# Kernel tuning notes

Hardware: AMD Instinct MI355X
Metric: run time of the kernel (lower is better)

The kernel has to match this reference:

```python
import jax, jax.numpy as jnp
import numpy as np

B, T, F, H = 64, 2048, 128, 32  # batch, seq_len, input_features, lstm hidden


def setup_inputs() -> dict:
    key = jax.random.key(0)
    ks = jax.random.split(key, 4)
    X = jax.random.normal(ks[0], (B, T, F), dtype=jnp.float32)
    # combined gate weights, order (i, f, g, o) as in flax.linen.LSTMCell
    Wx = jax.random.normal(ks[1], (F, 4 * H), dtype=jnp.float32) / np.float32(np.sqrt(F))
    Wh = jax.random.normal(ks[2], (H, 4 * H), dtype=jnp.float32) / np.float32(np.sqrt(H))
    b = jnp.zeros((4 * H,), dtype=jnp.float32)
    Wd = jax.random.normal(ks[3], (H, 1), dtype=jnp.float32) / np.float32(np.sqrt(H))
    bd = jnp.zeros((1,), dtype=jnp.float32)
    return {"X": X, "Wx": Wx, "Wh": Wh, "b": b, "Wd": Wd, "bd": bd}


def reference(X, Wx, Wh, b, Wd, bd):
    # Precompute input->gate projections for all timesteps in one GEMM.
    xg = jnp.einsum('btf,fg->btg', X, Wx) + b  # [B, T, 4H]

    def step(carry, xg_t):
        c, h = carry
        g = xg_t + h @ Wh  # [B, 4H]
        i, f, gc, o = jnp.split(g, 4, axis=-1)
        c = jax.nn.sigmoid(f) * c + jax.nn.sigmoid(i) * jnp.tanh(gc)
        h = jax.nn.sigmoid(o) * jnp.tanh(c)
        return (c, h), None

    zeros = jnp.zeros((X.shape[0], H), X.dtype)
    (c_T, h_T), _ = jax.lax.scan(step, (zeros, zeros), jnp.swapaxes(xg, 0, 1))
    # Dense(1) applied to outputs, then last timestep selected == Dense on h_T
    return h_T @ Wd + bd  # [B, 1]
```

## Files before the change

### kernel.cpp

```cpp
#include <hip/hip_runtime.h>
#include <math.h>

#define BB 64
#define TT 2048
#define FF 128
#define HH 32
#define GG 128

#define S1f (-1.4426950408889634f)
#define S2f (-2.8853900817779268f)

typedef _Float16 half2_t __attribute__((ext_vector_type(2)));

__device__ __forceinline__ unsigned h2u(half2_t v) {
    unsigned u; __builtin_memcpy(&u, &v, 4); return u;
}
__device__ __forceinline__ half2_t u2h(unsigned u) {
    half2_t v; __builtin_memcpy(&v, &u, 4); return v;
}
__device__ __forceinline__ half2_t pkrtz(float a, float b) {
    auto r = __builtin_amdgcn_cvt_pkrtz(a, b);
    half2_t v; __builtin_memcpy(&v, &r, 4); return v;
}
__device__ __forceinline__ float rcp_(float x) { return __builtin_amdgcn_rcpf(x); }
__device__ __forceinline__ float exp2_(float x) { return __builtin_amdgcn_exp2f(x); }

#define DPP_(x, ctrl) \
    ((unsigned)__builtin_amdgcn_mov_dpp((int)(x), (ctrl), 0xF, 0xF, true))
#define CTRL_XOR1 0xB1
#define CTRL_XOR2 0x4E
#define CTRL_ROR4 0x124
#define CTRL_ROR8 0x128
#define SWZ16_(x) ((unsigned)__builtin_amdgcn_ds_swizzle((int)(x), 0x401F))

#if __has_builtin(__builtin_amdgcn_permlane16_swap)
#define HAVE_PL16 1
#else
#define HAVE_PL16 0
#endif

__device__ __forceinline__ void gather_tree(unsigned v0, unsigned g[16]) {
    unsigned v1 = DPP_(v0, CTRL_XOR2);
#if HAVE_PL16
    auto sw = __builtin_amdgcn_permlane16_swap(v0, v1, false, false);
    unsigned s0 = (unsigned)sw[0], s1 = (unsigned)sw[1];
    g[0] = s0;
    g[1] = s1;
    g[2] = DPP_(s0, CTRL_XOR2);
    g[3] = DPP_(s1, CTRL_XOR2);
#else
    g[0] = v0;
    g[1] = v1;
    g[2] = SWZ16_(v0);
    g[3] = SWZ16_(v1);
#endif
#pragma unroll
    for (int r = 0; r < 4; ++r) g[4 + r] = DPP_(g[r], CTRL_ROR4);
#pragma unroll
    for (int r = 0; r < 8; ++r) g[8 + r] = DPP_(g[r], CTRL_ROR8);
}

__global__ __launch_bounds__(256) void xg_gemm(const float* __restrict__ X,
                                               const float* __restrict__ Wx,
                                               const float* __restrict__ bias,
                                               float* __restrict__ xgT) {
    __shared__ float XL[64 * 32];
    __shared__ float WL[32 * 128];
    const int tid = threadIdx.x;
    const int row0 = blockIdx.x * 64;
    const int j0 = (tid & 15) * 8;
    const int r0 = (tid >> 4) * 4;

    float acc[4][8];
#pragma unroll
    for (int r = 0; r < 4; ++r)
#pragma unroll
        for (int jj = 0; jj < 8; ++jj) acc[r][jj] = 0.f;

    for (int f0 = 0; f0 < FF; f0 += 32) {
        __syncthreads();
        {
            const float4* src = (const float4*)(Wx + f0 * GG);
            float4* dst = (float4*)WL;
            dst[tid]       = src[tid];
            dst[tid + 256] = src[tid + 256];
            dst[tid + 512] = src[tid + 512];
            dst[tid + 768] = src[tid + 768];
        }
        {
            int lin = tid * 4;
            int row = lin >> 5;
            int fi  = lin & 31;
            ((float4*)XL)[tid] =
                *(const float4*)(X + (size_t)(row0 + row) * FF + f0 + fi);
            lin = (tid + 256) * 4;
            row = lin >> 5;
            fi  = lin & 31;
            ((float4*)XL)[tid + 256] =
                *(const float4*)(X + (size_t)(row0 + row) * FF + f0 + fi);
        }
        __syncthreads();
#pragma unroll 4
        for (int fi = 0; fi < 32; ++fi) {
            float xv[4];
#pragma unroll
            for (int r = 0; r < 4; ++r) xv[r] = XL[(r0 + r) * 32 + fi];
            float4 w0 = *(float4*)&WL[fi * GG + j0];
            float4 w1 = *(float4*)&WL[fi * GG + j0 + 4];
            float w[8] = {w0.x, w0.y, w0.z, w0.w, w1.x, w1.y, w1.z, w1.w};
#pragma unroll
            for (int r = 0; r < 4; ++r)
#pragma unroll
                for (int jj = 0; jj < 8; ++jj)
                    acc[r][jj] = fmaf(xv[r], w[jj], acc[r][jj]);
        }
    }
    const int b  = row0 >> 11;
    const int t0 = (row0 & 2047) + r0;
    float bl[8];
#pragma unroll
    for (int jj = 0; jj < 8; ++jj) bl[jj] = bias[j0 + jj];
#pragma unroll
    for (int jj = 0; jj < 8; ++jj) {
        const int j = j0 + jj;
        const float sc = (j >= 64 && j < 96) ? S2f : S1f;
        float4 o;
        o.x = (acc[0][jj] + bl[jj]) * sc;
        o.y = (acc[1][jj] + bl[jj]) * sc;
        o.z = (acc[2][jj] + bl[jj]) * sc;
        o.w = (acc[3][jj] + bl[jj]) * sc;
        *(float4*)(xgT + ((size_t)b * GG + j) * TT + t0) = o;
    }
}

__global__ __launch_bounds__(64) void lstm_rec(const float* __restrict__ xgT,
                                               const float* __restrict__ Wh,
                                               const float* __restrict__ Wd,
                                               const float* __restrict__ bd,
                                               float* __restrict__ out) {
    const int l = threadIdx.x;
    const int m = l & 31;
    const bool lo = (l < HH);
    const int b = blockIdx.x;

    unsigned iv[16];
    gather_tree((unsigned)m, iv);

    const float scx = S1f;
    const float scy = lo ? S2f : S1f;
    half2_t whx[16], why[16];
#pragma unroll
    for (int r = 0; r < 16; ++r) {
        const int p  = (int)(iv[r] & 31u);
        const int p2 = p ^ 1;
        whx[r] = pkrtz(Wh[p * GG + l] * scx,       Wh[p2 * GG + l] * scx);
        why[r] = pkrtz(Wh[p * GG + l + 64] * scy,  Wh[p2 * GG + l + 64] * scy);
    }

    const float A1 = lo ? 2.f : 1.f;
    const float B1 = lo ? -1.f : 0.f;

    float h = 0.f;
    float c = 0.f;

    const float* pX = xgT + ((size_t)b * GG + l) * TT;
    const float* pY = xgT + ((size_t)b * GG + l + 64) * TT;

    float4 curX = *(const float4*)(pX);
    float4 curY = *(const float4*)(pY);
    float4 nxtX = *(const float4*)(pX + 4);
    float4 nxtY = *(const float4*)(pY + 4);

    auto step = [&](float xi, float xy) __attribute__((always_inline)) {
        unsigned hn = DPP_(__float_as_uint(h), CTRL_XOR1);
        unsigned g0 = h2u(pkrtz(h, __uint_as_float(hn)));
        unsigned g[16];
        gather_tree(g0, g);

        float ax[4] = {xi, 0.f, 0.f, 0.f};
        float ay[4] = {xy, 0.f, 0.f, 0.f};
#pragma unroll
        for (int r = 0; r < 16; ++r) {
            half2_t hp = u2h(g[r]);
            ax[r & 3] = __builtin_amdgcn_fdot2(hp, whx[r], ax[r & 3], false);
            ay[r & 3] = __builtin_amdgcn_fdot2(hp, why[r], ay[r & 3], false);
        }
        float a0 = (ax[0] + ax[1]) + (ax[2] + ax[3]);
        float a1 = (ay[0] + ay[1]) + (ay[2] + ay[3]);

        float act0 = rcp_(1.f + exp2_(a0));
        float act1 = fmaf(A1, rcp_(1.f + exp2_(a1)), B1);

        auto pq = __builtin_amdgcn_permlane32_swap(__float_as_uint(act0),
                                                   __float_as_uint(act1), false, false);
        auto uv = __builtin_amdgcn_permlane32_swap(__float_as_uint(act1),
                                                   __float_as_uint(act0), false, false);
        float p = __uint_as_float(pq[0]);
        float q = __uint_as_float(pq[1]);
        float u = __uint_as_float(uv[0]);
        float v = __uint_as_float(uv[1]);

        float f_all = lo ? q : act0;
        float o_all = lo ? v : act1;
        c = fmaf(f_all, c, u * p);
        float tc = fmaf(2.f, rcp_(1.f + exp2_(c * S2f)), -1.f);
        h = o_all * tc;
    };

#pragma unroll 1
    for (int t4 = 0; t4 < TT; t4 += 4) {
        float4 uX = curX, uY = curY;
        curX = nxtX; curY = nxtY;
        if (t4 + 8 < TT) {
            nxtX = *(const float4*)(pX + t4 + 8);
            nxtY = *(const float4*)(pY + t4 + 8);
        }
        step(uX.x, uY.x);
        step(uX.y, uY.y);
        step(uX.z, uY.z);
        step(uX.w, uY.w);
    }

    float contrib = h * Wd[m];
#pragma unroll
    for (int off = 32; off >= 1; off >>= 1)
        contrib += __shfl_xor(contrib, off, 64);
    if (l == 0) out[b] = fmaf(0.5f, contrib, bd[0]);
}

extern "C" void kernel_launch(void* const* d_in, const int* in_sizes, int n_in,
                              void* d_out, int out_size, void* d_ws, size_t ws_size,
                              hipStream_t stream) {
    const float* X    = (const float*)d_in[0];
    const float* Wx   = (const float*)d_in[1];
    const float* Wh   = (const float*)d_in[2];
    const float* bias = (const float*)d_in[3];
    const float* Wd   = (const float*)d_in[4];
    const float* bd   = (const float*)d_in[5];
    float* out = (float*)d_out;
    float* xgT = (float*)d_ws;

    hipLaunchKernelGGL(xg_gemm, dim3((BB * TT) / 64), dim3(256), 0, stream,
                       X, Wx, bias, xgT);
    hipLaunchKernelGGL(lstm_rec, dim3(BB), dim3(64), 0, stream,
                       xgT, Wh, Wd, bd, out);
}
```

Before: 500.2 us.

## Interleave two batch recurrences per wavefront and pack gate inputs as fp16 pairs

Each 64-lane block now runs the LSTM recurrence for two batch elements and interleaves their matvec and activation phases. The aim is to hide the serial latency chain of each timestep (DPP gathers, dot products, transcendental ops, permlane swaps) behind independent work from the other sequence. The GEMM kernel now writes the precomputed gate inputs as packed fp16 pairs (X and Y gate halves in one 32-bit word), which halves workspace traffic, and its column mapping is changed to match. The costs are half as many blocks (32 waves on a large GPU), more register pressure, and lower precision of the stored gate inputs.

```diff
diff --git a/kernel.cpp b/kernel.cpp
--- a/kernel.cpp
+++ b/kernel.cpp
@@ -63,12 +63,12 @@
 __global__ __launch_bounds__(256) void xg_gemm(const float* __restrict__ X,
                                                const float* __restrict__ Wx,
                                                const float* __restrict__ bias,
-                                               float* __restrict__ xgT) {
+                                               unsigned* __restrict__ xg2) {
     __shared__ float XL[64 * 32];
     __shared__ float WL[32 * 128];
     const int tid = threadIdx.x;
     const int row0 = blockIdx.x * 64;
-    const int j0 = (tid & 15) * 8;
+    const int j0 = (tid & 15) * 4;
     const int r0 = (tid >> 4) * 4;
 
     float acc[4][8];
@@ -106,7 +106,7 @@
 #pragma unroll
             for (int r = 0; r < 4; ++r) xv[r] = XL[(r0 + r) * 32 + fi];
             float4 w0 = *(float4*)&WL[fi * GG + j0];
-            float4 w1 = *(float4*)&WL[fi * GG + j0 + 4];
+            float4 w1 = *(float4*)&WL[fi * GG + j0 + 64];
             float w[8] = {w0.x, w0.y, w0.z, w0.w, w1.x, w1.y, w1.z, w1.w};
 #pragma unroll
             for (int r = 0; r < 4; ++r)
@@ -117,23 +117,22 @@
     }
     const int b  = row0 >> 11;
     const int t0 = (row0 & 2047) + r0;
-    float bl[8];
-#pragma unroll
-    for (int jj = 0; jj < 8; ++jj) bl[jj] = bias[j0 + jj];
-#pragma unroll
-    for (int jj = 0; jj < 8; ++jj) {
+#pragma unroll
+    for (int jj = 0; jj < 4; ++jj) {
         const int j = j0 + jj;
-        const float sc = (j >= 64 && j < 96) ? S2f : S1f;
-        float4 o;
-        o.x = (acc[0][jj] + bl[jj]) * sc;
-        o.y = (acc[1][jj] + bl[jj]) * sc;
-        o.z = (acc[2][jj] + bl[jj]) * sc;
-        o.w = (acc[3][jj] + bl[jj]) * sc;
-        *(float4*)(xgT + ((size_t)b * GG + j) * TT + t0) = o;
-    }
-}
-
-__global__ __launch_bounds__(64) void lstm_rec(const float* __restrict__ xgT,
+        const float bX = bias[j];
+        const float bY = bias[j + 64];
+        const float sY = (j < 32) ? S2f : S1f;
+        uint4 o;
+        o.x = h2u(pkrtz((acc[0][jj] + bX) * S1f, (acc[0][jj + 4] + bY) * sY));
+        o.y = h2u(pkrtz((acc[1][jj] + bX) * S1f, (acc[1][jj + 4] + bY) * sY));
+        o.z = h2u(pkrtz((acc[2][jj] + bX) * S1f, (acc[2][jj + 4] + bY) * sY));
+        o.w = h2u(pkrtz((acc[3][jj] + bX) * S1f, (acc[3][jj + 4] + bY) * sY));
+        *(uint4*)(xg2 + (size_t)(b * 64 + j) * TT + t0) = o;
+    }
+}
+
+__global__ __launch_bounds__(64) void lstm_rec(const unsigned* __restrict__ xg2,
                                                const float* __restrict__ Wh,
                                                const float* __restrict__ Wd,
                                                const float* __restrict__ bd,
@@ -141,7 +140,7 @@
     const int l = threadIdx.x;
     const int m = l & 31;
     const bool lo = (l < HH);
-    const int b = blockIdx.x;
+    const int b0 = blockIdx.x * 2;
 
     unsigned iv[16];
     gather_tree((unsigned)m, iv);
@@ -160,37 +159,39 @@
     const float A1 = lo ? 2.f : 1.f;
     const float B1 = lo ? -1.f : 0.f;
 
-    float h = 0.f;
-    float c = 0.f;
-
-    const float* pX = xgT + ((size_t)b * GG + l) * TT;
-    const float* pY = xgT + ((size_t)b * GG + l + 64) * TT;
-
-    float4 curX = *(const float4*)(pX);
-    float4 curY = *(const float4*)(pY);
-    float4 nxtX = *(const float4*)(pX + 4);
-    float4 nxtY = *(const float4*)(pY + 4);
-
-    auto step = [&](float xi, float xy) __attribute__((always_inline)) {
-        unsigned hn = DPP_(__float_as_uint(h), CTRL_XOR1);
-        unsigned g0 = h2u(pkrtz(h, __uint_as_float(hn)));
+    float hA = 0.f, cA = 0.f, hB = 0.f, cB = 0.f;
+
+    const unsigned* pA = xg2 + (size_t)(b0 * 64 + l) * TT;
+    const unsigned* pB = xg2 + (size_t)((b0 + 1) * 64 + l) * TT;
+
+    uint4 curA = *(const uint4*)(pA);
+    uint4 curB = *(const uint4*)(pB);
+    uint4 nxtA = *(const uint4*)(pA + 4);
+    uint4 nxtB = *(const uint4*)(pB + 4);
+
+    auto matvec = [&](float hq, unsigned xin, float& a0, float& a1)
+        __attribute__((always_inline)) {
+        unsigned hn = DPP_(__float_as_uint(hq), CTRL_XOR1);
+        unsigned g0 = h2u(pkrtz(hq, __uint_as_float(hn)));
         unsigned g[16];
         gather_tree(g0, g);
-
-        float ax[4] = {xi, 0.f, 0.f, 0.f};
-        float ay[4] = {xy, 0.f, 0.f, 0.f};
+        half2_t xv = u2h(xin);
+        float ax[4] = {(float)xv[0], 0.f, 0.f, 0.f};
+        float ay[4] = {(float)xv[1], 0.f, 0.f, 0.f};
 #pragma unroll
         for (int r = 0; r < 16; ++r) {
             half2_t hp = u2h(g[r]);
             ax[r & 3] = __builtin_amdgcn_fdot2(hp, whx[r], ax[r & 3], false);
             ay[r & 3] = __builtin_amdgcn_fdot2(hp, why[r], ay[r & 3], false);
         }
-        float a0 = (ax[0] + ax[1]) + (ax[2] + ax[3]);
-        float a1 = (ay[0] + ay[1]) + (ay[2] + ay[3]);
-
+        a0 = (ax[0] + ax[1]) + (ax[2] + ax[3]);
+        a1 = (ay[0] + ay[1]) + (ay[2] + ay[3]);
+    };
+
+    auto actupd = [&](float& hq, float& cq, float a0, float a1)
+        __attribute__((always_inline)) {
         float act0 = rcp_(1.f + exp2_(a0));
         float act1 = fmaf(A1, rcp_(1.f + exp2_(a1)), B1);
-
         auto pq = __builtin_amdgcn_permlane32_swap(__float_as_uint(act0),
                                                    __float_as_uint(act1), false, false);
         auto uv = __builtin_amdgcn_permlane32_swap(__float_as_uint(act1),
@@ -199,33 +200,55 @@
         float q = __uint_as_float(pq[1]);
         float u = __uint_as_float(uv[0]);
         float v = __uint_as_float(uv[1]);
-
         float f_all = lo ? q : act0;
         float o_all = lo ? v : act1;
-        c = fmaf(f_all, c, u * p);
-        float tc = fmaf(2.f, rcp_(1.f + exp2_(c * S2f)), -1.f);
-        h = o_all * tc;
+        cq = fmaf(f_all, cq, u * p);
+        float tc = fmaf(2.f, rcp_(1.f + exp2_(cq * S2f)), -1.f);
+        hq = o_all * tc;
     };
+
+    float a0A, a1A, a0B, a1B;
+    matvec(hA, curA.x, a0A, a1A);
 
 #pragma unroll 1
     for (int t4 = 0; t4 < TT; t4 += 4) {
-        float4 uX = curX, uY = curY;
-        curX = nxtX; curY = nxtY;
+        uint4 uA = curA, uB = curB;
+        curA = nxtA; curB = nxtB;
         if (t4 + 8 < TT) {
-            nxtX = *(const float4*)(pX + t4 + 8);
-            nxtY = *(const float4*)(pY + t4 + 8);
-        }
-        step(uX.x, uY.x);
-        step(uX.y, uY.y);
-        step(uX.z, uY.z);
-        step(uX.w, uY.w);
-    }
-
-    float contrib = h * Wd[m];
-#pragma unroll
-    for (int off = 32; off >= 1; off >>= 1)
-        contrib += __shfl_xor(contrib, off, 64);
-    if (l == 0) out[b] = fmaf(0.5f, contrib, bd[0]);
+            nxtA = *(const uint4*)(pA + t4 + 8);
+            nxtB = *(const uint4*)(pB + t4 + 8);
+        }
+        matvec(hB, uB.x, a0B, a1B);
+        actupd(hA, cA, a0A, a1A);
+        actupd(hB, cB, a0B, a1B);
+        matvec(hA, uA.y, a0A, a1A);
+        matvec(hB, uB.y, a0B, a1B);
+        actupd(hA, cA, a0A, a1A);
+        actupd(hB, cB, a0B, a1B);
+        matvec(hA, uA.z, a0A, a1A);
+        matvec(hB, uB.z, a0B, a1B);
+        actupd(hA, cA, a0A, a1A);
+        actupd(hB, cB, a0B, a1B);
+        matvec(hA, uA.w, a0A, a1A);
+        matvec(hB, uB.w, a0B, a1B);
+        actupd(hA, cA, a0A, a1A);
+        actupd(hB, cB, a0B, a1B);
+        if (t4 + 4 < TT)
+            matvec(hA, curA.x, a0A, a1A);
+    }
+
+    const float wd = Wd[m];
+    float ca = hA * wd;
+    float cb = hB * wd;
+#pragma unroll
+    for (int off = 32; off >= 1; off >>= 1) {
+        ca += __shfl_xor(ca, off, 64);
+        cb += __shfl_xor(cb, off, 64);
+    }
+    if (l == 0) {
+        out[b0]     = fmaf(0.5f, ca, bd[0]);
+        out[b0 + 1] = fmaf(0.5f, cb, bd[0]);
+    }
 }
 
 extern "C" void kernel_launch(void* const* d_in, const int* in_sizes, int n_in,
@@ -238,10 +261,10 @@
     const float* Wd   = (const float*)d_in[4];
     const float* bd   = (const float*)d_in[5];
     float* out = (float*)d_out;
-    float* xgT = (float*)d_ws;
+    unsigned* xg2 = (unsigned*)d_ws;
 
     hipLaunchKernelGGL(xg_gemm, dim3((BB * TT) / 64), dim3(256), 0, stream,
-                       X, Wx, bias, xgT);
-    hipLaunchKernelGGL(lstm_rec, dim3(BB), dim3(64), 0, stream,
-                       xgT, Wh, Wd, bd, out);
-}
+                       X, Wx, bias, xg2);
+    hipLaunchKernelGGL(lstm_rec, dim3(BB / 2), dim3(64), 0, stream,
+                       xg2, Wh, Wd, bd, out);
+}
```

After: 784.4 us. 56.8% more time.

## Pack two batches per wave, one hidden unit per lane, fp16 gate inputs

Applied to the files above, without the earlier changes.

The recurrence kernel now maps one hidden unit per lane and handles two batch rows per 64-lane wave, so each lane computes all four gates itself. This removes the permlane32 swaps at the cost of twice the dot-product work per lane and half as many blocks (32 instead of 64). The GEMM now writes the precomputed gate inputs as packed fp16 pairs laid out per hidden unit over time, which halves the bytes streamed by the recurrence but lowers the precision of the gate inputs. The longer per-step chain of dot products per lane may lengthen the serial critical path.

```diff
diff --git a/kernel.cpp b/kernel.cpp
--- a/kernel.cpp
+++ b/kernel.cpp
@@ -63,12 +63,12 @@
 __global__ __launch_bounds__(256) void xg_gemm(const float* __restrict__ X,
                                                const float* __restrict__ Wx,
                                                const float* __restrict__ bias,
-                                               float* __restrict__ xgT) {
+                                               unsigned* __restrict__ xgP) {
     __shared__ float XL[64 * 32];
     __shared__ float WL[32 * 128];
     const int tid = threadIdx.x;
     const int row0 = blockIdx.x * 64;
-    const int j0 = (tid & 15) * 8;
+    const int m0 = (tid & 15) * 2;
     const int r0 = (tid >> 4) * 4;
 
     float acc[4][8];
@@ -105,9 +105,11 @@
             float xv[4];
 #pragma unroll
             for (int r = 0; r < 4; ++r) xv[r] = XL[(r0 + r) * 32 + fi];
-            float4 w0 = *(float4*)&WL[fi * GG + j0];
-            float4 w1 = *(float4*)&WL[fi * GG + j0 + 4];
-            float w[8] = {w0.x, w0.y, w0.z, w0.w, w1.x, w1.y, w1.z, w1.w};
+            float2 wI = *(float2*)&WL[fi * GG + m0];
+            float2 wF = *(float2*)&WL[fi * GG + m0 + 32];
+            float2 wG = *(float2*)&WL[fi * GG + m0 + 64];
+            float2 wO = *(float2*)&WL[fi * GG + m0 + 96];
+            float w[8] = {wI.x, wI.y, wF.x, wF.y, wG.x, wG.y, wO.x, wO.y};
 #pragma unroll
             for (int r = 0; r < 4; ++r)
 #pragma unroll
@@ -117,115 +119,119 @@
     }
     const int b  = row0 >> 11;
     const int t0 = (row0 & 2047) + r0;
-    float bl[8];
-#pragma unroll
-    for (int jj = 0; jj < 8; ++jj) bl[jj] = bias[j0 + jj];
-#pragma unroll
-    for (int jj = 0; jj < 8; ++jj) {
-        const int j = j0 + jj;
-        const float sc = (j >= 64 && j < 96) ? S2f : S1f;
-        float4 o;
-        o.x = (acc[0][jj] + bl[jj]) * sc;
-        o.y = (acc[1][jj] + bl[jj]) * sc;
-        o.z = (acc[2][jj] + bl[jj]) * sc;
-        o.w = (acc[3][jj] + bl[jj]) * sc;
-        *(float4*)(xgT + ((size_t)b * GG + j) * TT + t0) = o;
-    }
-}
-
-__global__ __launch_bounds__(64) void lstm_rec(const float* __restrict__ xgT,
+#pragma unroll
+    for (int mm = 0; mm < 2; ++mm) {
+        const int m = m0 + mm;
+        const float bI = bias[m];
+        const float bF = bias[m + 32];
+        const float bG = bias[m + 64];
+        const float bO = bias[m + 96];
+        unsigned w0[4], w1[4];
+#pragma unroll
+        for (int r = 0; r < 4; ++r) {
+            w0[r] = h2u(pkrtz((acc[r][0 + mm] + bI) * S1f,
+                              (acc[r][2 + mm] + bF) * S1f));
+            w1[r] = h2u(pkrtz((acc[r][4 + mm] + bG) * S2f,
+                              (acc[r][6 + mm] + bO) * S1f));
+        }
+        unsigned* dst = xgP + ((size_t)(b * HH + m) * TT + t0) * 2;
+        *(uint4*)(dst)     = make_uint4(w0[0], w1[0], w0[1], w1[1]);
+        *(uint4*)(dst + 4) = make_uint4(w0[2], w1[2], w0[3], w1[3]);
+    }
+}
+
+__global__ __launch_bounds__(64) void lstm_rec(const unsigned* __restrict__ xgP,
                                                const float* __restrict__ Wh,
                                                const float* __restrict__ Wd,
                                                const float* __restrict__ bd,
                                                float* __restrict__ out) {
     const int l = threadIdx.x;
     const int m = l & 31;
-    const bool lo = (l < HH);
-    const int b = blockIdx.x;
+    const int grp = l >> 5;
+    const int b = blockIdx.x * 2 + grp;
 
     unsigned iv[16];
     gather_tree((unsigned)m, iv);
 
-    const float scx = S1f;
-    const float scy = lo ? S2f : S1f;
-    half2_t whx[16], why[16];
+    half2_t whI[16], whF[16], whG[16], whO[16];
 #pragma unroll
     for (int r = 0; r < 16; ++r) {
         const int p  = (int)(iv[r] & 31u);
         const int p2 = p ^ 1;
-        whx[r] = pkrtz(Wh[p * GG + l] * scx,       Wh[p2 * GG + l] * scx);
-        why[r] = pkrtz(Wh[p * GG + l + 64] * scy,  Wh[p2 * GG + l + 64] * scy);
-    }
-
-    const float A1 = lo ? 2.f : 1.f;
-    const float B1 = lo ? -1.f : 0.f;
+        whI[r] = pkrtz(Wh[p * GG + m]      * S1f, Wh[p2 * GG + m]      * S1f);
+        whF[r] = pkrtz(Wh[p * GG + m + 32] * S1f, Wh[p2 * GG + m + 32] * S1f);
+        whG[r] = pkrtz(Wh[p * GG + m + 64] * S2f, Wh[p2 * GG + m + 64] * S2f);
+        whO[r] = pkrtz(Wh[p * GG + m + 96] * S1f, Wh[p2 * GG + m + 96] * S1f);
+    }
 
     float h = 0.f;
     float c = 0.f;
 
-    const float* pX = xgT + ((size_t)b * GG + l) * TT;
-    const float* pY = xgT + ((size_t)b * GG + l + 64) * TT;
-
-    float4 curX = *(const float4*)(pX);
-    float4 curY = *(const float4*)(pY);
-    float4 nxtX = *(const float4*)(pX + 4);
-    float4 nxtY = *(const float4*)(pY + 4);
-
-    auto step = [&](float xi, float xy) __attribute__((always_inline)) {
+    const uint4* pX = (const uint4*)(xgP + (size_t)(b * HH + m) * TT * 2);
+    uint4 cur0 = pX[0];
+    uint4 cur1 = pX[1];
+    uint4 nxt0 = pX[2];
+    uint4 nxt1 = pX[3];
+
+    auto step = [&](unsigned wIF, unsigned wGO) __attribute__((always_inline)) {
         unsigned hn = DPP_(__float_as_uint(h), CTRL_XOR1);
         unsigned g0 = h2u(pkrtz(h, __uint_as_float(hn)));
         unsigned g[16];
         gather_tree(g0, g);
 
-        float ax[4] = {xi, 0.f, 0.f, 0.f};
-        float ay[4] = {xy, 0.f, 0.f, 0.f};
-#pragma unroll
-        for (int r = 0; r < 16; ++r) {
-            half2_t hp = u2h(g[r]);
-            ax[r & 3] = __builtin_amdgcn_fdot2(hp, whx[r], ax[r & 3], false);
-            ay[r & 3] = __builtin_amdgcn_fdot2(hp, why[r], ay[r & 3], false);
-        }
-        float a0 = (ax[0] + ax[1]) + (ax[2] + ax[3]);
-        float a1 = (ay[0] + ay[1]) + (ay[2] + ay[3]);
-
-        float act0 = rcp_(1.f + exp2_(a0));
-        float act1 = fmaf(A1, rcp_(1.f + exp2_(a1)), B1);
-
-        auto pq = __builtin_amdgcn_permlane32_swap(__float_as_uint(act0),
-                                                   __float_as_uint(act1), false, false);
-        auto uv = __builtin_amdgcn_permlane32_swap(__float_as_uint(act1),
-                                                   __float_as_uint(act0), false, false);
-        float p = __uint_as_float(pq[0]);
-        float q = __uint_as_float(pq[1]);
-        float u = __uint_as_float(uv[0]);
-        float v = __uint_as_float(uv[1]);
-
-        float f_all = lo ? q : act0;
-        float o_all = lo ? v : act1;
-        c = fmaf(f_all, c, u * p);
+        half2_t xIF = u2h(wIF);
+        half2_t xGO = u2h(wGO);
+        float aI0 = (float)xIF[0], aI1 = 0.f;
+        float aF0 = (float)xIF[1], aF1 = 0.f;
+        float aG0 = (float)xGO[0], aG1 = 0.f;
+        float aO0 = (float)xGO[1], aO1 = 0.f;
+#pragma unroll
+        for (int r = 0; r < 16; r += 2) {
+            half2_t hp0 = u2h(g[r]);
+            half2_t hp1 = u2h(g[r + 1]);
+            aI0 = __builtin_amdgcn_fdot2(hp0, whI[r],     aI0, false);
+            aI1 = __builtin_amdgcn_fdot2(hp1, whI[r + 1], aI1, false);
+            aF0 = __builtin_amdgcn_fdot2(hp0, whF[r],     aF0, false);
+            aF1 = __builtin_amdgcn_fdot2(hp1, whF[r + 1], aF1, false);
+            aG0 = __builtin_amdgcn_fdot2(hp0, whG[r],     aG0, false);
+            aG1 = __builtin_amdgcn_fdot2(hp1, whG[r + 1], aG1, false);
+            aO0 = __builtin_amdgcn_fdot2(hp0, whO[r],     aO0, false);
+            aO1 = __builtin_amdgcn_fdot2(hp1, whO[r + 1], aO1, false);
+        }
+        float aI = aI0 + aI1;
+        float aF = aF0 + aF1;
+        float aG = aG0 + aG1;
+        float aO = aO0 + aO1;
+
+        float si = rcp_(1.f + exp2_(aI));
+        float sf = rcp_(1.f + exp2_(aF));
+        float tg = fmaf(2.f, rcp_(1.f + exp2_(aG)), -1.f);
+        float so = rcp_(1.f + exp2_(aO));
+
+        c = fmaf(sf, c, si * tg);
         float tc = fmaf(2.f, rcp_(1.f + exp2_(c * S2f)), -1.f);
-        h = o_all * tc;
+        h = so * tc;
     };
 
 #pragma unroll 1
     for (int t4 = 0; t4 < TT; t4 += 4) {
-        float4 uX = curX, uY = curY;
-        curX = nxtX; curY = nxtY;
+        uint4 u0 = cur0, u1 = cur1;
+        cur0 = nxt0; cur1 = nxt1;
         if (t4 + 8 < TT) {
-            nxtX = *(const float4*)(pX + t4 + 8);
-            nxtY = *(const float4*)(pY + t4 + 8);
-        }
-        step(uX.x, uY.x);
-        step(uX.y, uY.y);
-        step(uX.z, uY.z);
-        step(uX.w, uY.w);
-    }
-
-    float contrib = h * Wd[m];
-#pragma unroll
-    for (int off = 32; off >= 1; off >>= 1)
-        contrib += __shfl_xor(contrib, off, 64);
-    if (l == 0) out[b] = fmaf(0.5f, contrib, bd[0]);
+            nxt0 = pX[t4 / 2 + 4];
+            nxt1 = pX[t4 / 2 + 5];
+        }
+        step(u0.x, u0.y);
+        step(u0.z, u0.w);
+        step(u1.x, u1.y);
+        step(u1.z, u1.w);
+    }
+
+    float ca = h * Wd[m];
+#pragma unroll
+    for (int off = 16; off >= 1; off >>= 1)
+        ca += __shfl_xor(ca, off, 64);
+    if (m == 0) out[b] = ca + bd[0];
 }
 
 extern "C" void kernel_launch(void* const* d_in, const int* in_sizes, int n_in,
@@ -238,10 +244,10 @@
     const float* Wd   = (const float*)d_in[4];
     const float* bd   = (const float*)d_in[5];
     float* out = (float*)d_out;
-    float* xgT = (float*)d_ws;
+    unsigned* xgP = (unsigned*)d_ws;
 
     hipLaunchKernelGGL(xg_gemm, dim3((BB * TT) / 64), dim3(256), 0, stream,
-                       X, Wx, bias, xgT);
-    hipLaunchKernelGGL(lstm_rec, dim3(BB), dim3(64), 0, stream,
-                       xgT, Wh, Wd, bd, out);
-}
+                       X, Wx, bias, xgP);
+    hipLaunchKernelGGL(lstm_rec, dim3(BB / 2), dim3(64), 0, stream,
+                       xgP, Wh, Wd, bd, out);
+}
```

New measurement: 611.0 us. 22.1% more time.

## Fuse input projection into recurrent kernel with producer waves and LDS double buffer

Applied to the files above, without the earlier changes.

Replaces the separate GEMM plus recurrence kernels with one kernel per batch element. Three producer waves compute the input-gate projections per 64-step chunk using fp16 dot2 and write them packed as half2 into a double-buffered LDS array. Meanwhile wave 0 runs the LSTM recurrence from the previous chunk. This removes the global write and read of the full xg tensor and one launch, at the cost of per-chunk block barriers, reduced precision of xg, and producer waves sharing the CU with the latency-critical recurrence wave.

```diff
diff --git a/kernel.cpp b/kernel.cpp
--- a/kernel.cpp
+++ b/kernel.cpp
@@ -6,6 +6,8 @@
 #define FF 128
 #define HH 32
 #define GG 128
+#define CH 64
+#define NCH (TT / CH)
 
 #define S1f (-1.4426950408889634f)
 #define S2f (-2.8853900817779268f)
@@ -24,6 +26,9 @@
 }
 __device__ __forceinline__ float rcp_(float x) { return __builtin_amdgcn_rcpf(x); }
 __device__ __forceinline__ float exp2_(float x) { return __builtin_amdgcn_exp2f(x); }
+__device__ __forceinline__ float fdot2_(half2_t a, half2_t b, float c) {
+    return __builtin_amdgcn_fdot2(a, b, c, false);
+}
 
 #define DPP_(x, ctrl) \
     ((unsigned)__builtin_amdgcn_mov_dpp((int)(x), (ctrl), 0xF, 0xF, true))
@@ -60,137 +65,84 @@
     for (int r = 0; r < 8; ++r) g[8 + r] = DPP_(g[r], CTRL_ROR8);
 }
 
-__global__ __launch_bounds__(256) void xg_gemm(const float* __restrict__ X,
-                                               const float* __restrict__ Wx,
-                                               const float* __restrict__ bias,
-                                               float* __restrict__ xgT) {
-    __shared__ float XL[64 * 32];
-    __shared__ float WL[32 * 128];
+__global__ __launch_bounds__(256) void lstm_fused(const float* __restrict__ X,
+                                                  const float* __restrict__ Wx,
+                                                  const float* __restrict__ Wh,
+                                                  const float* __restrict__ bias,
+                                                  const float* __restrict__ Wd,
+                                                  const float* __restrict__ bd,
+                                                  float* __restrict__ out) {
+    __shared__ unsigned xbuf[2][CH][64];
+    __shared__ uint4 wxl[64][32];
+
     const int tid = threadIdx.x;
-    const int row0 = blockIdx.x * 64;
-    const int j0 = (tid & 15) * 8;
-    const int r0 = (tid >> 4) * 4;
-
-    float acc[4][8];
-#pragma unroll
-    for (int r = 0; r < 4; ++r)
-#pragma unroll
-        for (int jj = 0; jj < 8; ++jj) acc[r][jj] = 0.f;
-
-    for (int f0 = 0; f0 < FF; f0 += 32) {
-        __syncthreads();
-        {
-            const float4* src = (const float4*)(Wx + f0 * GG);
-            float4* dst = (float4*)WL;
-            dst[tid]       = src[tid];
-            dst[tid + 256] = src[tid + 256];
-            dst[tid + 512] = src[tid + 512];
-            dst[tid + 768] = src[tid + 768];
+    const int wid = tid >> 6;
+    const int l   = tid & 63;
+    const int m32 = l & 31;
+    const bool lo = (l < HH);
+    const int b   = blockIdx.x;
+
+#pragma unroll
+    for (int j = 0; j < 8; ++j) {
+        int idx = tid + j * 256;
+        int r = idx >> 5, m = idx & 31;
+        const float* w0 = Wx + (size_t)(2 * r) * GG + m;
+        const float* w1 = w0 + GG;
+        uint4 e;
+        e.x = h2u(pkrtz(w0[0],  w1[0]));
+        e.y = h2u(pkrtz(w0[32], w1[32]));
+        e.z = h2u(pkrtz(w0[64], w1[64]));
+        e.w = h2u(pkrtz(w0[96], w1[96]));
+        wxl[r][m] = e;
+    }
+
+    float h = 0.f, c = 0.f;
+    half2_t whx[16], why[16];
+    float A1 = 1.f, B1 = 0.f;
+    float bI = 0.f, bF = 0.f, bG = 0.f, bO = 0.f;
+    const int dtp = l >> 5;
+
+    if (wid == 0) {
+        unsigned iv[16];
+        gather_tree((unsigned)m32, iv);
+        const float scx = S1f;
+        const float scy = lo ? S2f : S1f;
+#pragma unroll
+        for (int r = 0; r < 16; ++r) {
+            const int p  = (int)(iv[r] & 31u);
+            const int p2 = p ^ 1;
+            whx[r] = pkrtz(Wh[p * GG + l] * scx,      Wh[p2 * GG + l] * scx);
+            why[r] = pkrtz(Wh[p * GG + l + 64] * scy, Wh[p2 * GG + l + 64] * scy);
         }
-        {
-            int lin = tid * 4;
-            int row = lin >> 5;
-            int fi  = lin & 31;
-            ((float4*)XL)[tid] =
-                *(const float4*)(X + (size_t)(row0 + row) * FF + f0 + fi);
-            lin = (tid + 256) * 4;
-            row = lin >> 5;
-            fi  = lin & 31;
-            ((float4*)XL)[tid + 256] =
-                *(const float4*)(X + (size_t)(row0 + row) * FF + f0 + fi);
-        }
-        __syncthreads();
-#pragma unroll 4
-        for (int fi = 0; fi < 32; ++fi) {
-            float xv[4];
-#pragma unroll
-            for (int r = 0; r < 4; ++r) xv[r] = XL[(r0 + r) * 32 + fi];
-            float4 w0 = *(float4*)&WL[fi * GG + j0];
-            float4 w1 = *(float4*)&WL[fi * GG + j0 + 4];
-            float w[8] = {w0.x, w0.y, w0.z, w0.w, w1.x, w1.y, w1.z, w1.w};
-#pragma unroll
-            for (int r = 0; r < 4; ++r)
-#pragma unroll
-                for (int jj = 0; jj < 8; ++jj)
-                    acc[r][jj] = fmaf(xv[r], w[jj], acc[r][jj]);
-        }
-    }
-    const int b  = row0 >> 11;
-    const int t0 = (row0 & 2047) + r0;
-    float bl[8];
-#pragma unroll
-    for (int jj = 0; jj < 8; ++jj) bl[jj] = bias[j0 + jj];
-#pragma unroll
-    for (int jj = 0; jj < 8; ++jj) {
-        const int j = j0 + jj;
-        const float sc = (j >= 64 && j < 96) ? S2f : S1f;
-        float4 o;
-        o.x = (acc[0][jj] + bl[jj]) * sc;
-        o.y = (acc[1][jj] + bl[jj]) * sc;
-        o.z = (acc[2][jj] + bl[jj]) * sc;
-        o.w = (acc[3][jj] + bl[jj]) * sc;
-        *(float4*)(xgT + ((size_t)b * GG + j) * TT + t0) = o;
-    }
-}
-
-__global__ __launch_bounds__(64) void lstm_rec(const float* __restrict__ xgT,
-                                               const float* __restrict__ Wh,
-                                               const float* __restrict__ Wd,
-                                               const float* __restrict__ bd,
-                                               float* __restrict__ out) {
-    const int l = threadIdx.x;
-    const int m = l & 31;
-    const bool lo = (l < HH);
-    const int b = blockIdx.x;
-
-    unsigned iv[16];
-    gather_tree((unsigned)m, iv);
-
-    const float scx = S1f;
-    const float scy = lo ? S2f : S1f;
-    half2_t whx[16], why[16];
-#pragma unroll
-    for (int r = 0; r < 16; ++r) {
-        const int p  = (int)(iv[r] & 31u);
-        const int p2 = p ^ 1;
-        whx[r] = pkrtz(Wh[p * GG + l] * scx,       Wh[p2 * GG + l] * scx);
-        why[r] = pkrtz(Wh[p * GG + l + 64] * scy,  Wh[p2 * GG + l + 64] * scy);
-    }
-
-    const float A1 = lo ? 2.f : 1.f;
-    const float B1 = lo ? -1.f : 0.f;
-
-    float h = 0.f;
-    float c = 0.f;
-
-    const float* pX = xgT + ((size_t)b * GG + l) * TT;
-    const float* pY = xgT + ((size_t)b * GG + l + 64) * TT;
-
-    float4 curX = *(const float4*)(pX);
-    float4 curY = *(const float4*)(pY);
-    float4 nxtX = *(const float4*)(pX + 4);
-    float4 nxtY = *(const float4*)(pY + 4);
-
-    auto step = [&](float xi, float xy) __attribute__((always_inline)) {
+        A1 = lo ? 2.f : 1.f;
+        B1 = lo ? -1.f : 0.f;
+    } else {
+        bI = bias[m32];
+        bF = bias[m32 + 32];
+        bG = bias[m32 + 64];
+        bO = bias[m32 + 96];
+    }
+
+    auto step = [&](unsigned w) __attribute__((always_inline)) {
+        half2_t xv = u2h(w);
+        float xi = (float)xv[0];
+        float xy = (float)xv[1];
         unsigned hn = DPP_(__float_as_uint(h), CTRL_XOR1);
         unsigned g0 = h2u(pkrtz(h, __uint_as_float(hn)));
         unsigned g[16];
         gather_tree(g0, g);
-
         float ax[4] = {xi, 0.f, 0.f, 0.f};
         float ay[4] = {xy, 0.f, 0.f, 0.f};
 #pragma unroll
         for (int r = 0; r < 16; ++r) {
             half2_t hp = u2h(g[r]);
-            ax[r & 3] = __builtin_amdgcn_fdot2(hp, whx[r], ax[r & 3], false);
-            ay[r & 3] = __builtin_amdgcn_fdot2(hp, why[r], ay[r & 3], false);
+            ax[r & 3] = fdot2_(hp, whx[r], ax[r & 3]);
+            ay[r & 3] = fdot2_(hp, why[r], ay[r & 3]);
         }
         float a0 = (ax[0] + ax[1]) + (ax[2] + ax[3]);
         float a1 = (ay[0] + ay[1]) + (ay[2] + ay[3]);
-
         float act0 = rcp_(1.f + exp2_(a0));
         float act1 = fmaf(A1, rcp_(1.f + exp2_(a1)), B1);
-
         auto pq = __builtin_amdgcn_permlane32_swap(__float_as_uint(act0),
                                                    __float_as_uint(act1), false, false);
         auto uv = __builtin_amdgcn_permlane32_swap(__float_as_uint(act1),
@@ -199,7 +151,6 @@
         float q = __uint_as_float(pq[1]);
         float u = __uint_as_float(uv[0]);
         float v = __uint_as_float(uv[1]);
-
         float f_all = lo ? q : act0;
         float o_all = lo ? v : act1;
         c = fmaf(f_all, c, u * p);
@@ -207,25 +158,62 @@
         h = o_all * tc;
     };
 
+    for (int k = 0; k <= NCH; ++k) {
+        __syncthreads();
+        if (wid == 0) {
+            if (k == 0) continue;
+            const unsigned* col = &xbuf[(k - 1) & 1][0][l];
+            unsigned c0 = col[0], c1 = col[64], c2 = col[128], c3 = col[192];
 #pragma unroll 1
-    for (int t4 = 0; t4 < TT; t4 += 4) {
-        float4 uX = curX, uY = curY;
-        curX = nxtX; curY = nxtY;
-        if (t4 + 8 < TT) {
-            nxtX = *(const float4*)(pX + t4 + 8);
-            nxtY = *(const float4*)(pY + t4 + 8);
+            for (int g4 = 0; g4 < CH; g4 += 4) {
+                unsigned n0 = 0, n1 = 0, n2 = 0, n3 = 0;
+                if (g4 + 4 < CH) {
+                    const unsigned* nc = col + (g4 + 4) * 64;
+                    n0 = nc[0]; n1 = nc[64]; n2 = nc[128]; n3 = nc[192];
+                }
+                step(c0); step(c1); step(c2); step(c3);
+                c0 = n0; c1 = n1; c2 = n2; c3 = n3;
+            }
+        } else if (k < NCH) {
+            const int t0 = k * CH;
+            unsigned (*ob)[64] = xbuf[k & 1];
+            for (int tt = t0 + (wid - 1) * 2 + dtp; tt < t0 + CH; tt += 6) {
+                const float4* xr = (const float4*)(X + ((size_t)b * TT + tt) * FF);
+                float aI = bI, aF = bF, aG = bG, aO = bO;
+#pragma unroll 4
+                for (int kk = 0; kk < 16; ++kk) {
+                    float4 xa = xr[2 * kk];
+                    float4 xb = xr[2 * kk + 1];
+                    half2_t p0 = pkrtz(xa.x, xa.y);
+                    half2_t p1 = pkrtz(xa.z, xa.w);
+                    half2_t p2 = pkrtz(xb.x, xb.y);
+                    half2_t p3 = pkrtz(xb.z, xb.w);
+                    uint4 w0 = wxl[4 * kk + 0][m32];
+                    uint4 w1 = wxl[4 * kk + 1][m32];
+                    uint4 w2 = wxl[4 * kk + 2][m32];
+                    uint4 w3 = wxl[4 * kk + 3][m32];
+                    aI = fdot2_(p0, u2h(w0.x), aI); aF = fdot2_(p0, u2h(w0.y), aF);
+                    aG = fdot2_(p0, u2h(w0.z), aG); aO = fdot2_(p0, u2h(w0.w), aO);
+                    aI = fdot2_(p1, u2h(w1.x), aI); aF = fdot2_(p1, u2h(w1.y), aF);
+                    aG = fdot2_(p1, u2h(w1.z), aG); aO = fdot2_(p1, u2h(w1.w), aO);
+                    aI = fdot2_(p2, u2h(w2.x), aI); aF = fdot2_(p2, u2h(w2.y), aF);
+                    aG = fdot2_(p2, u2h(w2.z), aG); aO = fdot2_(p2, u2h(w2.w), aO);
+                    aI = fdot2_(p3, u2h(w3.x), aI); aF = fdot2_(p3, u2h(w3.y), aF);
+                    aG = fdot2_(p3, u2h(w3.z), aG); aO = fdot2_(p3, u2h(w3.w), aO);
+                }
+                ob[tt - t0][m32]      = h2u(pkrtz(aI * S1f, aG * S2f));
+                ob[tt - t0][m32 + 32] = h2u(pkrtz(aF * S1f, aO * S1f));
+            }
         }
-        step(uX.x, uY.x);
-        step(uX.y, uY.y);
-        step(uX.z, uY.z);
-        step(uX.w, uY.w);
-    }
-
-    float contrib = h * Wd[m];
-#pragma unroll
-    for (int off = 32; off >= 1; off >>= 1)
-        contrib += __shfl_xor(contrib, off, 64);
-    if (l == 0) out[b] = fmaf(0.5f, contrib, bd[0]);
+    }
+
+    if (wid == 0) {
+        float ca = h * Wd[m32];
+#pragma unroll
+        for (int off = 32; off >= 1; off >>= 1)
+            ca += __shfl_xor(ca, off, 64);
+        if (l == 0) out[b] = fmaf(0.5f, ca, bd[0]);
+    }
 }
 
 extern "C" void kernel_launch(void* const* d_in, const int* in_sizes, int n_in,
@@ -238,10 +226,7 @@
     const float* Wd   = (const float*)d_in[4];
     const float* bd   = (const float*)d_in[5];
     float* out = (float*)d_out;
-    float* xgT = (float*)d_ws;
-
-    hipLaunchKernelGGL(xg_gemm, dim3((BB * TT) / 64), dim3(256), 0, stream,
-                       X, Wx, bias, xgT);
-    hipLaunchKernelGGL(lstm_rec, dim3(BB), dim3(64), 0, stream,
-                       xgT, Wh, Wd, bd, out);
-}
+
+    hipLaunchKernelGGL(lstm_fused, dim3(BB), dim3(256), 0, stream,
+                       X, Wx, Wh, bias, Wd, bd, out);
+}
```

New measurement: 646.9 us. 29.3% more time.
